# Optimization experiments

Hardware: AMD Instinct MI355X
Metric: run time of the kernel (lower is better)

## Reference

```python
import jax, jax.numpy as jnp
import numpy as np

B, T, D = 128, 512, 512
K = 64  # memory slots per bank


def setup_inputs() -> dict:
    key = jax.random.key(0)
    ks = jax.random.split(key, 8)
    stdv = 1.0 / np.sqrt(D)
    return {
        "x": jax.random.normal(ks[0], (B, T, D), jnp.float32),
        "Amem": jax.random.uniform(ks[1], (K, D), jnp.float32, -stdv, stdv),
        "Nmem": jax.random.uniform(ks[2], (K, D), jnp.float32, -stdv, stdv),
        "W_mu": jax.random.normal(ks[3], (D, D), jnp.float32) * 0.02,
        "b_mu": jnp.zeros((D,), jnp.float32),
        "W_var": jax.random.normal(ks[4], (D, D), jnp.float32) * 0.02,
        "b_var": jnp.zeros((D,), jnp.float32),
        # reparameterization noise (torch.randn_like(std)), shape of N_aug: [B//2, T, D]
        "epsilon": jax.random.normal(ks[5], (B // 2, T, D), jnp.float32),
    }


def _memory(data, mem):
    # UR-DMU / DA-MIST Memory_Bank: sigmoid attention over memory slots
    att = jax.nn.sigmoid(jnp.einsum('btd,kd->btk', data, mem)
                         / jnp.sqrt(jnp.asarray(mem.shape[-1], data.dtype)))
    topv, _ = jax.lax.top_k(att, mem.shape[0] // 16 + 1)   # [b,t,k']
    t_att = topv.mean(-1)                                  # [b,t]
    aug = jnp.einsum('btk,kd->btd', att, mem)              # [b,t,d]
    return t_att, aug


def _l2norm(v):
    return v / jnp.linalg.norm(v, axis=-1, keepdims=True)


def _gather_mean(feats, idx):
    # feats [b,t,d], idx [b,k] -> mean over gathered snippets -> [b,d]
    return jnp.take_along_axis(feats, idx[:, :, None], axis=1).mean(1)


def reference(x, Amem, Nmem, W_mu, b_mu, W_var, b_var, epsilon):
    b, t, d = x.shape
    mid = b // 2
    N_x, A_x = x[:mid], x[mid:]

    A_att, A_aug = _memory(A_x, Amem)
    N_Aatt, N_Aaug = _memory(A_x, Nmem)
    A_Natt, A_Naug = _memory(N_x, Amem)
    N_att, N_aug = _memory(N_x, Nmem)

    k = t // 16 + 1
    _, A_idx = jax.lax.top_k(A_att, k)   # [mid,k]
    _, N_idx = jax.lax.top_k(N_att, k)
    _, P_idx = jax.lax.top_k(N_Aatt, k)

    negative_ax = _gather_mean(A_x, A_idx)
    anchor_nx = _gather_mean(N_x, N_idx)
    positive_nx = _gather_mean(A_x, P_idx)

    a, p, n = _l2norm(anchor_nx), _l2norm(positive_nx), _l2norm(negative_ax)
    # torch TripletMarginLoss: pairwise_distance adds eps=1e-6 elementwise
    d_ap = jnp.linalg.norm(a - p + 1e-6, axis=-1)
    d_an = jnp.linalg.norm(a - n + 1e-6, axis=-1)
    triplet = jnp.mean(jnp.maximum(d_ap - d_an + 1.0, 0.0))

    mu_fn = lambda h: h @ W_mu + b_mu
    var_fn = lambda h: h @ W_var + b_var

    N_aug_mu = mu_fn(N_aug)
    N_aug_var = var_fn(N_aug)
    N_aug_new = N_aug_mu + epsilon * jnp.sqrt(jnp.exp(N_aug_var))

    anchor_nx_new = _gather_mean(N_aug_new, N_idx)    # reshape(mid,1,-1).mean(1) is identity
    A_aug_new = mu_fn(A_aug)
    negative_ax_new = _gather_mean(A_aug_new, A_idx)

    kl_loss = jnp.mean(-0.5 * jnp.sum(1.0 + N_aug_var - N_aug_mu ** 2 - jnp.exp(N_aug_var), axis=1))

    A_Naug_mu = mu_fn(A_Naug)
    N_Aaug_mu = mu_fn(N_Aaug)

    distance = jnp.mean(jax.nn.relu(100.0
                                    - jnp.linalg.norm(negative_ax_new, axis=-1)
                                    + jnp.linalg.norm(anchor_nx_new, axis=-1)))

    F_M = jnp.concatenate(
        [x, jnp.concatenate([N_aug_new + A_Naug_mu, A_aug_new + N_Aaug_mu], axis=0)],
        axis=-1)  # [b,t,2d]

    return (F_M, triplet, kl_loss, distance, A_att, N_att, A_Natt, N_Aatt)
```

## Files before the change

### kernel.cpp

```cpp
#include <hip/hip_runtime.h>
#include <hip/hip_bf16.h>
#include <math.h>

typedef unsigned short u16;
typedef __attribute__((ext_vector_type(4))) float f32x4;
typedef __attribute__((ext_vector_type(8))) short s16x8;

#define O_FM    0ULL
#define O_TRIP  67108864ULL
#define O_KL    67108865ULL
#define O_DIST  67108866ULL
#define O_AATT  67108867ULL
#define O_NATT  67141635ULL
#define O_ANATT 67174403ULL
#define O_NAATT 67207171ULL

#define WS_ATTB  0ULL
#define WS_BCT   16777216ULL
#define WS_PVT   16908288ULL
#define WS_PAM   16973824ULL
#define WS_PNM   17104896ULL
#define WS_PNV   17235968ULL
#define WS_MBH   17367040ULL
#define WS_MBL   17498112ULL
#define WS_TATT  17629184ULL
#define WS_IDX   18022400ULL
#define WS_GATH  18053120ULL
#define WS_NORM  18446336ULL
#define WS_KL    18446848ULL
#define WS_TRIPB 18447360ULL
#define WS_SUM   18447616ULL

__device__ __forceinline__ u16 f2bf(float f) {
    union { float f; unsigned int u; } c; c.f = f;
    unsigned int r = c.u + 0x7fffu + ((c.u >> 16) & 1u);
    return (u16)(r >> 16);
}
__device__ __forceinline__ float bf2f(u16 h) {
    union { unsigned int u; float f; } c; c.u = ((unsigned int)h) << 16;
    return c.f;
}

__device__ __forceinline__ float blk_sum(float v, float* red) {
    #pragma unroll
    for (int o = 32; o; o >>= 1) v += __shfl_xor(v, o);
    int tid = threadIdx.x;
    if ((tid & 63) == 0) red[tid >> 6] = v;
    __syncthreads();
    float r = red[0] + red[1] + red[2] + red[3];
    __syncthreads();
    return r;
}

__device__ __forceinline__ float blk_sum8(float v, float* red, int tid) {
    #pragma unroll
    for (int o = 32; o; o >>= 1) v += __shfl_xor(v, o);
    if ((tid & 63) == 0) red[tid >> 6] = v;
    __syncthreads();
    float r = red[0];
    #pragma unroll
    for (int i = 1; i < 8; ++i) r += red[i];
    __syncthreads();
    return r;
}

__device__ __forceinline__ void stage32_512(const u16* __restrict__ g, int row0, int ld, int k0,
                                            u16* s, int tid) {
    const u16* src = g + (size_t)(row0 + (tid >> 2)) * ld + k0 + (tid & 3) * 8;
    __builtin_amdgcn_global_load_lds((const __attribute__((address_space(1))) void*)src,
                                     (__attribute__((address_space(3))) void*)(s + tid * 8),
                                     16, 0, 0);
}

__global__ __launch_bounds__(256) void k_pp(const float* __restrict__ Amem, const float* __restrict__ Nmem,
                                            const float* __restrict__ Wmu, const float* __restrict__ Wvar,
                                            char* __restrict__ ws) {
    __shared__ float mr[512];
    int bid = blockIdx.x, tid = threadIdx.x;
    if (bid < 256) {
        int i = bid * 256 + tid;
        if (i == 0) *(float*)(ws + WS_KL) = 0.f;
        if (i < 32768) ((float*)(ws + WS_SUM))[i] = 0.f;
        int k = i >> 9, d = i & 511;
        float v = (k < 64) ? Amem[(size_t)k * 512 + d] : Nmem[(size_t)(k - 64) * 512 + d];
        u16 h = f2bf(v);
        ((u16*)(ws + WS_MBH))[i] = h;
        ((u16*)(ws + WS_MBL))[i] = f2bf(v - bf2f(h));
        return;
    }
    int pb = bid - 256;
    float* pam = (float*)(ws + WS_PAM);
    float* pnm = (float*)(ws + WS_PNM);
    float* pnv = (float*)(ws + WS_PNV);
    u16* bct = (u16*)(ws + WS_BCT);
    u16* pvt = (u16*)(ws + WS_PVT);
    int mat = pb >> 6, k = pb & 63;
    const float* mrow = ((mat == 0) ? Amem : Nmem) + (size_t)k * 512;
    const float* W = (mat == 2) ? Wvar : Wmu;
    mr[tid] = mrow[tid]; mr[tid + 256] = mrow[tid + 256];
    __syncthreads();
    float s0 = 0.f, s1 = 0.f;
    for (int d = 0; d < 512; ++d) {
        float m = mr[d];
        s0 += m * W[(size_t)d * 512 + tid];
        s1 += m * W[(size_t)d * 512 + tid + 256];
    }
    if (mat == 0) {
        pam[(size_t)k * 512 + tid] = s0; pam[(size_t)k * 512 + tid + 256] = s1;
        bct[(size_t)tid * 128 + k] = f2bf(s0); bct[(size_t)(tid + 256) * 128 + k] = f2bf(s1);
    } else if (mat == 1) {
        pnm[(size_t)k * 512 + tid] = s0; pnm[(size_t)k * 512 + tid + 256] = s1;
        bct[(size_t)tid * 128 + 64 + k] = f2bf(s0); bct[(size_t)(tid + 256) * 128 + 64 + k] = f2bf(s1);
    } else {
        pnv[(size_t)k * 512 + tid] = s0; pnv[(size_t)k * 512 + tid + 256] = s1;
        pvt[(size_t)tid * 64 + k] = f2bf(s0); pvt[(size_t)(tid + 256) * 64 + k] = f2bf(s1);
    }
}

__global__ __launch_bounds__(512) void k_dots(const float* __restrict__ x, char* __restrict__ ws,
                                              float* __restrict__ out) {
    __shared__ u16 sXh[128 * 32];
    __shared__ u16 sXl[128 * 32];
    __shared__ u16 sBh[128 * 32];
    __shared__ u16 sBl[128 * 32];

    int tid = threadIdx.x;
    int row0 = blockIdx.x * 128;
    const u16* mbh = (const u16*)(ws + WS_MBH);
    const u16* mbl = (const u16*)(ws + WS_MBL);
    u16* attb = (u16*)(ws + WS_ATTB);
    int lane = tid & 63, wid = tid >> 6;
    int cl = lane & 15, rq = lane >> 4;

    f32x4 acc[8];
    #pragma unroll
    for (int i = 0; i < 8; ++i) acc[i] = (f32x4)0.f;

    for (int dc = 0; dc < 16; ++dc) {
        int d0 = dc * 32;
        {
            int r = tid >> 2, q4 = tid & 3;
            const float* sp = x + (size_t)(row0 + r) * 512 + d0 + q4 * 8;
            float* op = out + (size_t)(row0 + r) * 1024 + d0 + q4 * 8;
            f32x4 v0 = *(const f32x4*)(sp);
            f32x4 v1 = *(const f32x4*)(sp + 4);
            *(f32x4*)(op) = v0;
            *(f32x4*)(op + 4) = v1;
            s16x8 hs, ls;
            #pragma unroll
            for (int j = 0; j < 4; ++j) {
                u16 h0 = f2bf(v0[j]); hs[j] = (short)h0; ls[j] = (short)f2bf(v0[j] - bf2f(h0));
                u16 h1 = f2bf(v1[j]); hs[4 + j] = (short)h1; ls[4 + j] = (short)f2bf(v1[j] - bf2f(h1));
            }
            *(s16x8*)&sXh[r * 32 + q4 * 8] = hs;
            *(s16x8*)&sXl[r * 32 + q4 * 8] = ls;
        }
        stage32_512(mbh, 0, 512, d0, sBh, tid);
        stage32_512(mbl, 0, 512, d0, sBl, tid);
        __syncthreads();
        s16x8 axh = *(const s16x8*)&sXh[(wid * 16 + cl) * 32 + rq * 8];
        s16x8 axl = *(const s16x8*)&sXl[(wid * 16 + cl) * 32 + rq * 8];
        #pragma unroll
        for (int ni = 0; ni < 8; ++ni) {
            s16x8 bh = *(const s16x8*)&sBh[(ni * 16 + cl) * 32 + rq * 8];
            s16x8 bl = *(const s16x8*)&sBl[(ni * 16 + cl) * 32 + rq * 8];
            acc[ni] = __builtin_amdgcn_mfma_f32_16x16x32_bf16(axh, bh, acc[ni], 0, 0, 0);
            acc[ni] = __builtin_amdgcn_mfma_f32_16x16x32_bf16(axh, bl, acc[ni], 0, 0, 0);
            acc[ni] = __builtin_amdgcn_mfma_f32_16x16x32_bf16(axl, bh, acc[ni], 0, 0, 0);
        }
        __syncthreads();
    }

    #pragma unroll
    for (int ni = 0; ni < 8; ++ni) {
        #pragma unroll
        for (int q = 0; q < 4; ++q) {
            float logit = acc[ni][q] * 0.044194173824159216f;
            float av = 1.f / (1.f + expf(-logit));
            acc[ni][q] = av;
            attb[(size_t)(row0 + wid * 16 + rq * 4 + q) * 128 + ni * 16 + cl] = f2bf(av);
        }
    }

    unsigned long long gmask = 0xFFFFull << (lane & 48);
    float* tatt = (float*)(ws + WS_TATT);
    int half = row0 >> 15;
    #pragma unroll
    for (int q = 0; q < 4; ++q) {
        #pragma unroll
        for (int side = 0; side < 2; ++side) {
            float v0 = acc[side * 4 + 0][q], v1 = acc[side * 4 + 1][q];
            float v2 = acc[side * 4 + 2][q], v3 = acc[side * 4 + 3][q];
            float sum5 = 0.f;
            #pragma unroll
            for (int it = 0; it < 5; ++it) {
                float m = v0; int jm = 0;
                if (v1 > m) { m = v1; jm = 1; }
                if (v2 > m) { m = v2; jm = 2; }
                if (v3 > m) { m = v3; jm = 3; }
                float g = m;
                g = fmaxf(g, __shfl_xor(g, 1));
                g = fmaxf(g, __shfl_xor(g, 2));
                g = fmaxf(g, __shfl_xor(g, 4));
                g = fmaxf(g, __shfl_xor(g, 8));
                sum5 += g;
                unsigned long long bl = __ballot(m == g) & gmask;
                int owner = __ffsll(bl) - 1;
                if (lane == owner) {
                    if (jm == 0) v0 = -INFINITY;
                    else if (jm == 1) v1 = -INFINITY;
                    else if (jm == 2) v2 = -INFINITY;
                    else v3 = -INFINITY;
                }
            }
            if (cl == 0) {
                float tv = sum5 / 5.f;
                int lr = (row0 + wid * 16 + rq * 4 + q) & 32767;
                if (half) {
                    if (side == 0) { out[O_AATT + lr]  = tv; tatt[lr] = tv; }
                    else           { out[O_NAATT + lr] = tv; tatt[2 * 32768 + lr] = tv; }
                } else {
                    if (side == 0) { out[O_ANATT + lr] = tv; }
                    else           { out[O_NATT + lr]  = tv; tatt[32768 + lr] = tv; }
                }
            }
        }
    }
}

__global__ __launch_bounds__(256) void k_tg(const float* __restrict__ tatt, int* __restrict__ idx,
                                            const float* __restrict__ x, float* __restrict__ gath) {
    __shared__ float vals[512];
    __shared__ int il[40];
    int s = blockIdx.x >> 6, b = blockIdx.x & 63, tid = threadIdx.x;
    const float* src = tatt + (size_t)s * 32768 + b * 512;
    vals[tid] = src[tid]; vals[tid + 256] = src[tid + 256];
    __syncthreads();
    #pragma unroll
    for (int e = 0; e < 2; ++e) {
        int i = tid + e * 256;
        float v = vals[i];
        int rank = 0;
        for (int j = 0; j < 512; j += 4) {
            f32x4 w4 = *(const f32x4*)&vals[j];
            rank += (w4.x > v) || (w4.x == v && (j + 0) < i);
            rank += (w4.y > v) || (w4.y == v && (j + 1) < i);
            rank += (w4.z > v) || (w4.z == v && (j + 2) < i);
            rank += (w4.w > v) || (w4.w == v && (j + 3) < i);
        }
        if (rank < 33) { idx[(s * 64 + b) * 40 + rank] = i; il[rank] = i; }
    }
    __syncthreads();
    int srcb = (s == 1) ? b : 64 + b;
    const float* xb = x + (size_t)srcb * 262144;
    int d0 = tid * 2;
    float a0 = 0.f, a1 = 0.f;
    for (int i = 0; i < 33; ++i) {
        const float* p = xb + (size_t)il[i] * 512 + d0;
        a0 += p[0]; a1 += p[1];
    }
    gath[((size_t)s * 64 + b) * 512 + d0]     = a0 / 33.f;
    gath[((size_t)s * 64 + b) * 512 + d0 + 1] = a1 / 33.f;
}

__device__ __forceinline__ void body_G1(char* smem, int m0, int c0, int tid,
                                        const u16* __restrict__ attb, const u16* __restrict__ bct,
                                        const u16* __restrict__ pvt, const float* __restrict__ bmu,
                                        const float* __restrict__ bvar, const float* __restrict__ epsv,
                                        float* __restrict__ fm, float* __restrict__ klacc) {
    u16* sAA = (u16*)(smem);
    u16* sAN = (u16*)(smem + 8192);
    u16* sBA = (u16*)(smem + 16384);
    u16* sBN = (u16*)(smem + 24576);
    u16* sBV = (u16*)(smem + 32768);
    float* red = (float*)(smem + 40960);
    int lane = tid & 63, wid = tid >> 6;
    int wr = wid >> 2, wc = wid & 3;
    int cl = lane & 15, rq = lane >> 4;

    f32x4 aA[4][2], aN[4][2], aV[4][2];
    #pragma unroll
    for (int i = 0; i < 4; ++i)
        #pragma unroll
        for (int j = 0; j < 2; ++j) { aA[i][j] = (f32x4)0.f; aN[i][j] = (f32x4)0.f; aV[i][j] = (f32x4)0.f; }

    for (int kt = 0; kt < 2; ++kt) {
        stage32_512(attb, m0, 128, kt * 32, sAA, tid);
        stage32_512(attb, m0, 128, 64 + kt * 32, sAN, tid);
        stage32_512(bct, c0, 128, kt * 32, sBA, tid);
        stage32_512(bct, c0, 128, 64 + kt * 32, sBN, tid);
        stage32_512(pvt, c0, 64, kt * 32, sBV, tid);
        __syncthreads();
        s16x8 fA[4], fN[4], bA[2], bN[2], bV[2];
        #pragma unroll
        for (int i = 0; i < 4; ++i) {
            fA[i] = *(const s16x8*)&sAA[(wr * 64 + i * 16 + cl) * 32 + rq * 8];
            fN[i] = *(const s16x8*)&sAN[(wr * 64 + i * 16 + cl) * 32 + rq * 8];
        }
        #pragma unroll
        for (int n = 0; n < 2; ++n) {
            bA[n] = *(const s16x8*)&sBA[(wc * 32 + n * 16 + cl) * 32 + rq * 8];
            bN[n] = *(const s16x8*)&sBN[(wc * 32 + n * 16 + cl) * 32 + rq * 8];
            bV[n] = *(const s16x8*)&sBV[(wc * 32 + n * 16 + cl) * 32 + rq * 8];
        }
        #pragma unroll
        for (int mi = 0; mi < 4; ++mi)
            #pragma unroll
            for (int ni = 0; ni < 2; ++ni) {
                aA[mi][ni] = __builtin_amdgcn_mfma_f32_16x16x32_bf16(fA[mi], bA[ni], aA[mi][ni], 0, 0, 0);
                aN[mi][ni] = __builtin_amdgcn_mfma_f32_16x16x32_bf16(fN[mi], bN[ni], aN[mi][ni], 0, 0, 0);
                aV[mi][ni] = __builtin_amdgcn_mfma_f32_16x16x32_bf16(fN[mi], bV[ni], aV[mi][ni], 0, 0, 0);
            }
        __syncthreads();
    }

    float kll = 0.f;
    #pragma unroll
    for (int mi = 0; mi < 4; ++mi)
        #pragma unroll
        for (int ni = 0; ni < 2; ++ni) {
            int col = c0 + wc * 32 + ni * 16 + cl;
            int rowb = m0 + wr * 64 + mi * 16 + rq * 4;
            float bm = bmu[col], bv = bvar[col];
            #pragma unroll
            for (int q = 0; q < 4; ++q) {
                int row = rowb + q;
                float muN = aN[mi][ni][q] + bm;
                float var = aV[mi][ni][q] + bv;
                float ev = expf(var);
                float muA = aA[mi][ni][q] + bm;
                fm[(size_t)row * 1024 + 512 + col] =
                    muN + epsv[(size_t)row * 512 + col] * sqrtf(ev) + muA;
                kll += 1.f + var - muN * muN - ev;
            }
        }
    #pragma unroll
    for (int o = 32; o; o >>= 1) kll += __shfl_xor(kll, o);
    if (lane == 0) red[wid] = kll;
    __syncthreads();
    if (tid == 0) {
        float s = 0.f;
        #pragma unroll
        for (int i = 0; i < 8; ++i) s += red[i];
        atomicAdd(klacc, s);
    }
}

__device__ __forceinline__ void body_G3(char* smem, int m0, int c0, int tid,
                                        const u16* __restrict__ attb, const u16* __restrict__ bct,
                                        const float* __restrict__ bmu, float* __restrict__ fm) {
    u16* sA = (u16*)(smem);
    u16* sB = (u16*)(smem + 8192);
    int lane = tid & 63, wid = tid >> 6;
    int wr = wid >> 2, wc = wid & 3;
    int cl = lane & 15, rq = lane >> 4;

    f32x4 acc[4][2];
    #pragma unroll
    for (int i = 0; i < 4; ++i)
        #pragma unroll
        for (int j = 0; j < 2; ++j) acc[i][j] = (f32x4)0.f;

    for (int kt = 0; kt < 4; ++kt) {
        stage32_512(attb, 32768 + m0, 128, kt * 32, sA, tid);
        stage32_512(bct, c0, 128, kt * 32, sB, tid);
        __syncthreads();
        s16x8 fa[4], fb[2];
        #pragma unroll
        for (int i = 0; i < 4; ++i)
            fa[i] = *(const s16x8*)&sA[(wr * 64 + i * 16 + cl) * 32 + rq * 8];
        #pragma unroll
        for (int n = 0; n < 2; ++n)
            fb[n] = *(const s16x8*)&sB[(wc * 32 + n * 16 + cl) * 32 + rq * 8];
        #pragma unroll
        for (int mi = 0; mi < 4; ++mi)
            #pragma unroll
            for (int ni = 0; ni < 2; ++ni)
                acc[mi][ni] = __builtin_amdgcn_mfma_f32_16x16x32_bf16(fa[mi], fb[ni], acc[mi][ni], 0, 0, 0);
        __syncthreads();
    }
    #pragma unroll
    for (int mi = 0; mi < 4; ++mi)
        #pragma unroll
        for (int ni = 0; ni < 2; ++ni) {
            int col = c0 + wc * 32 + ni * 16 + cl;
            int rowb = 32768 + m0 + wr * 64 + mi * 16 + rq * 4;
            float bm2 = 2.f * bmu[col];
            #pragma unroll
            for (int q = 0; q < 4; ++q)
                fm[(size_t)(rowb + q) * 1024 + 512 + col] = acc[mi][ni][q] + bm2;
        }
}

__device__ __forceinline__ void body_g2a(char* smem, int blk, int tid,
                                         const int* __restrict__ idx, const u16* __restrict__ attb,
                                         const float* __restrict__ pnm, const float* __restrict__ pnv,
                                         const float* __restrict__ bmu, const float* __restrict__ bvar,
                                         const float* __restrict__ epsv, float* __restrict__ SUM) {
    float* arow = (float*)smem;
    int b = blk / 3, seg = blk % 3;
    float s0 = 0.f, s1 = 0.f;
    for (int i = seg * 11; i < seg * 11 + 11; ++i) {
        int t = idx[(64 + b) * 40 + i];
        size_t r = (size_t)b * 512 + t;
        __syncthreads();
        if (tid < 64) arow[tid] = bf2f(attb[r * 128 + 64 + tid]);
        __syncthreads();
        if (tid < 256) {
            float mu0 = bmu[tid], mu1 = bmu[tid + 256];
            float v0 = bvar[tid], v1 = bvar[tid + 256];
            for (int k = 0; k < 64; ++k) {
                float a = arow[k];
                mu0 += a * pnm[(size_t)k * 512 + tid];
                mu1 += a * pnm[(size_t)k * 512 + tid + 256];
                v0  += a * pnv[(size_t)k * 512 + tid];
                v1  += a * pnv[(size_t)k * 512 + tid + 256];
            }
            s0 += mu0 + bf2f(f2bf(0.f)) + epsv[r * 512 + tid]       * sqrtf(expf(v0));
            s1 += mu1 + epsv[r * 512 + tid + 256] * sqrtf(expf(v1));
        }
    }
    if (tid < 256) {
        atomicAdd(&SUM[(size_t)b * 512 + tid], s0);
        atomicAdd(&SUM[(size_t)b * 512 + tid + 256], s1);
    }
}

__device__ __forceinline__ void body_g2b(char* smem, int b, int tid,
                                         const int* __restrict__ idx, const u16* __restrict__ attb,
                                         const float* __restrict__ pam, const float* __restrict__ bmu,
                                         float* __restrict__ norms) {
    float* meanA = (float*)smem;
    float* red = (float*)(smem + 256);
    if (tid < 64) {
        float s = 0.f;
        for (int i = 0; i < 33; ++i) {
            int t = idx[b * 40 + i];
            s += bf2f(attb[(size_t)(32768 + b * 512 + t) * 128 + tid]);
        }
        meanA[tid] = s * (1.f / 33.f);
    }
    __syncthreads();
    float ssv = 0.f;
    if (tid < 256) {
        float s0 = bmu[tid], s1 = bmu[tid + 256];
        #pragma unroll 4
        for (int k = 0; k < 64; ++k) {
            float m = meanA[k];
            s0 += m * pam[(size_t)k * 512 + tid];
            s1 += m * pam[(size_t)k * 512 + tid + 256];
        }
        ssv = s0 * s0 + s1 * s1;
    }
    float ss = blk_sum8(ssv, red, tid);
    if (tid == 0) norms[64 + b] = sqrtf(ss);
}

__global__ __launch_bounds__(512) void k_post(const u16* __restrict__ attb, const u16* __restrict__ bct,
                                              const u16* __restrict__ pvt, const float* __restrict__ bmu,
                                              const float* __restrict__ bvar, const float* __restrict__ epsv,
                                              const int* __restrict__ idx, const float* __restrict__ pam,
                                              const float* __restrict__ pnm, const float* __restrict__ pnv,
                                              float* __restrict__ fm, float* __restrict__ klacc,
                                              float* __restrict__ SUM, float* __restrict__ norms) {
    __shared__ __align__(16) char smem[41024];
    int bid = blockIdx.x, tid = threadIdx.x;
    if (bid < 1024) {
        body_G1(smem, (bid >> 2) * 128, (bid & 3) * 128, tid, attb, bct, pvt, bmu, bvar, epsv, fm, klacc);
    } else if (bid < 2048) {
        int b2 = bid - 1024;
        body_G3(smem, (b2 >> 2) * 128, (b2 & 3) * 128, tid, attb, bct, bmu, fm);
    } else if (bid < 2240) {
        body_g2a(smem, bid - 2048, tid, idx, attb, pnm, pnv, bmu, bvar, epsv, SUM);
    } else {
        body_g2b(smem, bid - 2240, tid, idx, attb, pam, bmu, norms);
    }
}

__global__ __launch_bounds__(256) void k_nt(const float* __restrict__ SUM, const float* __restrict__ gath,
                                            float* __restrict__ norms, float* __restrict__ tripb) {
    __shared__ float red[8];
    int bid = blockIdx.x, tid = threadIdx.x;
    if (bid < 64) {
        int b = bid;
        float s0 = SUM[(size_t)b * 512 + tid] / 33.f;
        float s1 = SUM[(size_t)b * 512 + tid + 256] / 33.f;
        float ss = blk_sum(s0 * s0 + s1 * s1, red);
        if (tid == 0) norms[b] = sqrtf(ss);
    } else {
        int b = bid - 64;
        const float* a = gath + (size_t)(64 + b) * 512;
        const float* p = gath + (size_t)(128 + b) * 512;
        const float* n = gath + (size_t)(b) * 512;
        float a0 = a[tid], a1 = a[tid + 256];
        float p0 = p[tid], p1 = p[tid + 256];
        float n0 = n[tid], n1 = n[tid + 256];
        float na  = sqrtf(blk_sum(a0 * a0 + a1 * a1, red));
        float npv = sqrtf(blk_sum(p0 * p0 + p1 * p1, red));
        float nn  = sqrtf(blk_sum(n0 * n0 + n1 * n1, red));
        float e0 = a0 / na - p0 / npv + 1e-6f, e1 = a1 / na - p1 / npv + 1e-6f;
        float f0 = a0 / na - n0 / nn  + 1e-6f, f1 = a1 / na - n1 / nn  + 1e-6f;
        float dap = sqrtf(blk_sum(e0 * e0 + e1 * e1, red));
        float dan = sqrtf(blk_sum(f0 * f0 + f1 * f1, red));
        if (tid == 0) tripb[b] = fmaxf(dap - dan + 1.f, 0.f);
    }
}

__global__ __launch_bounds__(64) void k_final(const float* __restrict__ norms, const float* __restrict__ klacc,
                                              const float* __restrict__ tripb, float* __restrict__ out) {
    int tid = threadIdx.x;
    float v = fmaxf(100.f - norms[64 + tid] + norms[tid], 0.f);
    float t = tripb[tid];
    #pragma unroll
    for (int o = 32; o; o >>= 1) { v += __shfl_xor(v, o); t += __shfl_xor(t, o); }
    if (tid == 0) {
        out[O_DIST] = v / 64.f;
        out[O_TRIP] = t / 64.f;
        out[O_KL]   = -0.5f * (*klacc) / 32768.f;
    }
}

extern "C" void kernel_launch(void* const* d_in, const int* in_sizes, int n_in,
                              void* d_out, int out_size, void* d_ws, size_t ws_size,
                              hipStream_t stream) {
    const float* x    = (const float*)d_in[0];
    const float* Amem = (const float*)d_in[1];
    const float* Nmem = (const float*)d_in[2];
    const float* Wmu  = (const float*)d_in[3];
    const float* bmu  = (const float*)d_in[4];
    const float* Wvar = (const float*)d_in[5];
    const float* bvar = (const float*)d_in[6];
    const float* eps  = (const float*)d_in[7];
    float* out = (float*)d_out;
    char* ws = (char*)d_ws;
    const u16* attb  = (const u16*)(ws + WS_ATTB);
    const u16* bct   = (const u16*)(ws + WS_BCT);
    const u16* pvt   = (const u16*)(ws + WS_PVT);
    const float* pam = (const float*)(ws + WS_PAM);
    const float* pnm = (const float*)(ws + WS_PNM);
    const float* pnv = (const float*)(ws + WS_PNV);
    const int* idx   = (const int*)(ws + WS_IDX);

    k_pp<<<448, 256, 0, stream>>>(Amem, Nmem, Wmu, Wvar, ws);
    k_dots<<<512, 512, 0, stream>>>(x, ws, out);
    k_tg<<<192, 256, 0, stream>>>((const float*)(ws + WS_TATT), (int*)(ws + WS_IDX), x,
                                  (float*)(ws + WS_GATH));
    k_post<<<2304, 512, 0, stream>>>(attb, bct, pvt, bmu, bvar, eps, idx, pam, pnm, pnv,
                                     out, (float*)(ws + WS_KL), (float*)(ws + WS_SUM),
                                     (float*)(ws + WS_NORM));
    k_nt<<<128, 256, 0, stream>>>((const float*)(ws + WS_SUM), (const float*)(ws + WS_GATH),
                                  (float*)(ws + WS_NORM), (float*)(ws + WS_TRIPB));
    k_final<<<1, 64, 0, stream>>>((const float*)(ws + WS_NORM), (const float*)(ws + WS_KL),
                                  (const float*)(ws + WS_TRIPB), out);
}
```

Baseline: 272.4 us.

## Fuse norm, triplet and final reductions into k_post; widen k_dots K-chunk

Removes the k_nt and k_final launches. Per-batch norms now run in the last-arriving g2a block, found with an atomic counter; the triplet blocks are appended to k_post; and the final scalar reduction runs in the globally last block, selected by a second atomic counter. Separately, k_dots now stages 64-wide K chunks instead of 32, which halves the number of barrier iterations but doubles shared memory use. The changes save two launch gaps and some synchronisation, in exchange for atomics and threadfences in every k_post block and possible lower occupancy in k_dots.

```diff
diff --git a/kernel.cpp b/kernel.cpp
--- a/kernel.cpp
+++ b/kernel.cpp
@@ -30,6 +30,10 @@
 #define WS_KL    18446848ULL
 #define WS_TRIPB 18447360ULL
 #define WS_SUM   18447616ULL
+#define WS_CNTB  18578688ULL
+#define WS_GCNT  18578944ULL
+
+#define NPOST 2368
 
 __device__ __forceinline__ u16 f2bf(float f) {
     union { float f; unsigned int u; } c; c.f = f;
@@ -39,17 +43,6 @@
 __device__ __forceinline__ float bf2f(u16 h) {
     union { unsigned int u; float f; } c; c.u = ((unsigned int)h) << 16;
     return c.f;
-}
-
-__device__ __forceinline__ float blk_sum(float v, float* red) {
-    #pragma unroll
-    for (int o = 32; o; o >>= 1) v += __shfl_xor(v, o);
-    int tid = threadIdx.x;
-    if ((tid & 63) == 0) red[tid >> 6] = v;
-    __syncthreads();
-    float r = red[0] + red[1] + red[2] + red[3];
-    __syncthreads();
-    return r;
 }
 
 __device__ __forceinline__ float blk_sum8(float v, float* red, int tid) {
@@ -70,6 +63,16 @@
     __builtin_amdgcn_global_load_lds((const __attribute__((address_space(1))) void*)src,
                                      (__attribute__((address_space(3))) void*)(s + tid * 8),
                                      16, 0, 0);
+}
+
+__device__ __forceinline__ void stage64_512(const u16* __restrict__ g, int d0, u16* s, int tid) {
+    #pragma unroll
+    for (int j = 0; j < 2; ++j) {
+        const u16* src = g + (size_t)(j * 64 + (tid >> 3)) * 512 + d0 + (tid & 7) * 8;
+        __builtin_amdgcn_global_load_lds((const __attribute__((address_space(1))) void*)src,
+                                         (__attribute__((address_space(3))) void*)(s + j * 4096 + tid * 8),
+                                         16, 0, 0);
+    }
 }
 
 __global__ __launch_bounds__(256) void k_pp(const float* __restrict__ Amem, const float* __restrict__ Nmem,
@@ -79,7 +82,8 @@
     int bid = blockIdx.x, tid = threadIdx.x;
     if (bid < 256) {
         int i = bid * 256 + tid;
-        if (i == 0) *(float*)(ws + WS_KL) = 0.f;
+        if (i == 0) { *(float*)(ws + WS_KL) = 0.f; *(int*)(ws + WS_GCNT) = 0; }
+        if (bid == 0 && tid < 64) ((int*)(ws + WS_CNTB))[tid] = 0;
         if (i < 32768) ((float*)(ws + WS_SUM))[i] = 0.f;
         int k = i >> 9, d = i & 511;
         float v = (k < 64) ? Amem[(size_t)k * 512 + d] : Nmem[(size_t)(k - 64) * 512 + d];
@@ -119,10 +123,10 @@
 
 __global__ __launch_bounds__(512) void k_dots(const float* __restrict__ x, char* __restrict__ ws,
                                               float* __restrict__ out) {
-    __shared__ u16 sXh[128 * 32];
-    __shared__ u16 sXl[128 * 32];
-    __shared__ u16 sBh[128 * 32];
-    __shared__ u16 sBl[128 * 32];
+    __shared__ u16 sXh[128 * 64];
+    __shared__ u16 sXl[128 * 64];
+    __shared__ u16 sBh[128 * 64];
+    __shared__ u16 sBl[128 * 64];
 
     int tid = threadIdx.x;
     int row0 = blockIdx.x * 128;
@@ -136,37 +140,46 @@
     #pragma unroll
     for (int i = 0; i < 8; ++i) acc[i] = (f32x4)0.f;
 
-    for (int dc = 0; dc < 16; ++dc) {
-        int d0 = dc * 32;
+    for (int dc = 0; dc < 8; ++dc) {
+        int d0 = dc * 64;
         {
             int r = tid >> 2, q4 = tid & 3;
-            const float* sp = x + (size_t)(row0 + r) * 512 + d0 + q4 * 8;
-            float* op = out + (size_t)(row0 + r) * 1024 + d0 + q4 * 8;
+            const float* sp = x + (size_t)(row0 + r) * 512 + d0 + q4 * 16;
+            float* op = out + (size_t)(row0 + r) * 1024 + d0 + q4 * 16;
             f32x4 v0 = *(const f32x4*)(sp);
             f32x4 v1 = *(const f32x4*)(sp + 4);
-            *(f32x4*)(op) = v0;
-            *(f32x4*)(op + 4) = v1;
-            s16x8 hs, ls;
+            f32x4 v2 = *(const f32x4*)(sp + 8);
+            f32x4 v3 = *(const f32x4*)(sp + 12);
+            *(f32x4*)(op) = v0; *(f32x4*)(op + 4) = v1;
+            *(f32x4*)(op + 8) = v2; *(f32x4*)(op + 12) = v3;
+            s16x8 h0, l0, h1, l1;
             #pragma unroll
             for (int j = 0; j < 4; ++j) {
-                u16 h0 = f2bf(v0[j]); hs[j] = (short)h0; ls[j] = (short)f2bf(v0[j] - bf2f(h0));
-                u16 h1 = f2bf(v1[j]); hs[4 + j] = (short)h1; ls[4 + j] = (short)f2bf(v1[j] - bf2f(h1));
-            }
-            *(s16x8*)&sXh[r * 32 + q4 * 8] = hs;
-            *(s16x8*)&sXl[r * 32 + q4 * 8] = ls;
-        }
-        stage32_512(mbh, 0, 512, d0, sBh, tid);
-        stage32_512(mbl, 0, 512, d0, sBl, tid);
-        __syncthreads();
-        s16x8 axh = *(const s16x8*)&sXh[(wid * 16 + cl) * 32 + rq * 8];
-        s16x8 axl = *(const s16x8*)&sXl[(wid * 16 + cl) * 32 + rq * 8];
-        #pragma unroll
-        for (int ni = 0; ni < 8; ++ni) {
-            s16x8 bh = *(const s16x8*)&sBh[(ni * 16 + cl) * 32 + rq * 8];
-            s16x8 bl = *(const s16x8*)&sBl[(ni * 16 + cl) * 32 + rq * 8];
-            acc[ni] = __builtin_amdgcn_mfma_f32_16x16x32_bf16(axh, bh, acc[ni], 0, 0, 0);
-            acc[ni] = __builtin_amdgcn_mfma_f32_16x16x32_bf16(axh, bl, acc[ni], 0, 0, 0);
-            acc[ni] = __builtin_amdgcn_mfma_f32_16x16x32_bf16(axl, bh, acc[ni], 0, 0, 0);
+                u16 a = f2bf(v0[j]); h0[j] = (short)a; l0[j] = (short)f2bf(v0[j] - bf2f(a));
+                u16 b = f2bf(v1[j]); h0[4 + j] = (short)b; l0[4 + j] = (short)f2bf(v1[j] - bf2f(b));
+                u16 c = f2bf(v2[j]); h1[j] = (short)c; l1[j] = (short)f2bf(v2[j] - bf2f(c));
+                u16 d = f2bf(v3[j]); h1[4 + j] = (short)d; l1[4 + j] = (short)f2bf(v3[j] - bf2f(d));
+            }
+            *(s16x8*)&sXh[r * 64 + q4 * 16]     = h0;
+            *(s16x8*)&sXh[r * 64 + q4 * 16 + 8] = h1;
+            *(s16x8*)&sXl[r * 64 + q4 * 16]     = l0;
+            *(s16x8*)&sXl[r * 64 + q4 * 16 + 8] = l1;
+        }
+        stage64_512(mbh, d0, sBh, tid);
+        stage64_512(mbl, d0, sBl, tid);
+        __syncthreads();
+        #pragma unroll
+        for (int kk = 0; kk < 2; ++kk) {
+            s16x8 axh = *(const s16x8*)&sXh[(wid * 16 + cl) * 64 + kk * 32 + rq * 8];
+            s16x8 axl = *(const s16x8*)&sXl[(wid * 16 + cl) * 64 + kk * 32 + rq * 8];
+            #pragma unroll
+            for (int ni = 0; ni < 8; ++ni) {
+                s16x8 bh = *(const s16x8*)&sBh[(ni * 16 + cl) * 64 + kk * 32 + rq * 8];
+                s16x8 bl = *(const s16x8*)&sBl[(ni * 16 + cl) * 64 + kk * 32 + rq * 8];
+                acc[ni] = __builtin_amdgcn_mfma_f32_16x16x32_bf16(axh, bh, acc[ni], 0, 0, 0);
+                acc[ni] = __builtin_amdgcn_mfma_f32_16x16x32_bf16(axh, bl, acc[ni], 0, 0, 0);
+                acc[ni] = __builtin_amdgcn_mfma_f32_16x16x32_bf16(axl, bh, acc[ni], 0, 0, 0);
+            }
         }
         __syncthreads();
     }
@@ -416,7 +429,7 @@
                 v0  += a * pnv[(size_t)k * 512 + tid];
                 v1  += a * pnv[(size_t)k * 512 + tid + 256];
             }
-            s0 += mu0 + bf2f(f2bf(0.f)) + epsv[r * 512 + tid]       * sqrtf(expf(v0));
+            s0 += mu0 + epsv[r * 512 + tid]       * sqrtf(expf(v0));
             s1 += mu1 + epsv[r * 512 + tid + 256] * sqrtf(expf(v1));
         }
     }
@@ -456,14 +469,56 @@
     if (tid == 0) norms[64 + b] = sqrtf(ss);
 }
 
+__device__ __forceinline__ void body_norm2a(char* smem, int b, int tid,
+                                            const float* __restrict__ SUM, float* __restrict__ norms) {
+    float* red = (float*)smem;
+    float v = 0.f;
+    if (tid < 256) {
+        float s0 = SUM[(size_t)b * 512 + tid] / 33.f;
+        float s1 = SUM[(size_t)b * 512 + tid + 256] / 33.f;
+        v = s0 * s0 + s1 * s1;
+    }
+    float ss = blk_sum8(v, red, tid);
+    if (tid == 0) norms[b] = sqrtf(ss);
+}
+
+__device__ __forceinline__ void body_trip(char* smem, int b, int tid,
+                                          const float* __restrict__ gath, float* __restrict__ tripb) {
+    float* red = (float*)smem;
+    const float* a = gath + (size_t)(64 + b) * 512;
+    const float* p = gath + (size_t)(128 + b) * 512;
+    const float* n = gath + (size_t)(b) * 512;
+    float a0 = 0.f, a1 = 0.f, p0 = 0.f, p1 = 0.f, n0 = 0.f, n1 = 0.f;
+    if (tid < 256) {
+        a0 = a[tid]; a1 = a[tid + 256];
+        p0 = p[tid]; p1 = p[tid + 256];
+        n0 = n[tid]; n1 = n[tid + 256];
+    }
+    float na  = sqrtf(blk_sum8(tid < 256 ? a0 * a0 + a1 * a1 : 0.f, red, tid));
+    float npv = sqrtf(blk_sum8(tid < 256 ? p0 * p0 + p1 * p1 : 0.f, red, tid));
+    float nn  = sqrtf(blk_sum8(tid < 256 ? n0 * n0 + n1 * n1 : 0.f, red, tid));
+    float e0 = 0.f, e1 = 0.f, f0 = 0.f, f1 = 0.f;
+    if (tid < 256) {
+        e0 = a0 / na - p0 / npv + 1e-6f; e1 = a1 / na - p1 / npv + 1e-6f;
+        f0 = a0 / na - n0 / nn  + 1e-6f; f1 = a1 / na - n1 / nn  + 1e-6f;
+    }
+    float dap = sqrtf(blk_sum8(tid < 256 ? e0 * e0 + e1 * e1 : 0.f, red, tid));
+    float dan = sqrtf(blk_sum8(tid < 256 ? f0 * f0 + f1 * f1 : 0.f, red, tid));
+    if (tid == 0) tripb[b] = fmaxf(dap - dan + 1.f, 0.f);
+}
+
 __global__ __launch_bounds__(512) void k_post(const u16* __restrict__ attb, const u16* __restrict__ bct,
                                               const u16* __restrict__ pvt, const float* __restrict__ bmu,
                                               const float* __restrict__ bvar, const float* __restrict__ epsv,
                                               const int* __restrict__ idx, const float* __restrict__ pam,
                                               const float* __restrict__ pnm, const float* __restrict__ pnv,
+                                              const float* __restrict__ gath,
                                               float* __restrict__ fm, float* __restrict__ klacc,
-                                              float* __restrict__ SUM, float* __restrict__ norms) {
+                                              float* __restrict__ SUM, float* __restrict__ norms,
+                                              float* __restrict__ tripb, int* __restrict__ cntb,
+                                              int* __restrict__ gcnt, float* __restrict__ out) {
     __shared__ __align__(16) char smem[41024];
+    __shared__ int sflag;
     int bid = blockIdx.x, tid = threadIdx.x;
     if (bid < 1024) {
         body_G1(smem, (bid >> 2) * 128, (bid & 3) * 128, tid, attb, bct, pvt, bmu, bvar, epsv, fm, klacc);
@@ -471,52 +526,36 @@
         int b2 = bid - 1024;
         body_G3(smem, (b2 >> 2) * 128, (b2 & 3) * 128, tid, attb, bct, bmu, fm);
     } else if (bid < 2240) {
-        body_g2a(smem, bid - 2048, tid, idx, attb, pnm, pnv, bmu, bvar, epsv, SUM);
+        int blk = bid - 2048;
+        body_g2a(smem, blk, tid, idx, attb, pnm, pnv, bmu, bvar, epsv, SUM);
+        int b = blk / 3;
+        __threadfence();
+        __syncthreads();
+        if (tid == 0) sflag = (atomicAdd(&cntb[b], 1) == 2) ? 1 : 0;
+        __syncthreads();
+        if (sflag) { __threadfence(); body_norm2a(smem, b, tid, SUM, norms); }
+    } else if (bid < 2304) {
+        body_g2b(smem, bid - 2240, tid, idx, attb, pam, bmu, norms);
     } else {
-        body_g2b(smem, bid - 2240, tid, idx, attb, pam, bmu, norms);
-    }
-}
-
-__global__ __launch_bounds__(256) void k_nt(const float* __restrict__ SUM, const float* __restrict__ gath,
-                                            float* __restrict__ norms, float* __restrict__ tripb) {
-    __shared__ float red[8];
-    int bid = blockIdx.x, tid = threadIdx.x;
-    if (bid < 64) {
-        int b = bid;
-        float s0 = SUM[(size_t)b * 512 + tid] / 33.f;
-        float s1 = SUM[(size_t)b * 512 + tid + 256] / 33.f;
-        float ss = blk_sum(s0 * s0 + s1 * s1, red);
-        if (tid == 0) norms[b] = sqrtf(ss);
-    } else {
-        int b = bid - 64;
-        const float* a = gath + (size_t)(64 + b) * 512;
-        const float* p = gath + (size_t)(128 + b) * 512;
-        const float* n = gath + (size_t)(b) * 512;
-        float a0 = a[tid], a1 = a[tid + 256];
-        float p0 = p[tid], p1 = p[tid + 256];
-        float n0 = n[tid], n1 = n[tid + 256];
-        float na  = sqrtf(blk_sum(a0 * a0 + a1 * a1, red));
-        float npv = sqrtf(blk_sum(p0 * p0 + p1 * p1, red));
-        float nn  = sqrtf(blk_sum(n0 * n0 + n1 * n1, red));
-        float e0 = a0 / na - p0 / npv + 1e-6f, e1 = a1 / na - p1 / npv + 1e-6f;
-        float f0 = a0 / na - n0 / nn  + 1e-6f, f1 = a1 / na - n1 / nn  + 1e-6f;
-        float dap = sqrtf(blk_sum(e0 * e0 + e1 * e1, red));
-        float dan = sqrtf(blk_sum(f0 * f0 + f1 * f1, red));
-        if (tid == 0) tripb[b] = fmaxf(dap - dan + 1.f, 0.f);
-    }
-}
-
-__global__ __launch_bounds__(64) void k_final(const float* __restrict__ norms, const float* __restrict__ klacc,
-                                              const float* __restrict__ tripb, float* __restrict__ out) {
-    int tid = threadIdx.x;
-    float v = fmaxf(100.f - norms[64 + tid] + norms[tid], 0.f);
-    float t = tripb[tid];
-    #pragma unroll
-    for (int o = 32; o; o >>= 1) { v += __shfl_xor(v, o); t += __shfl_xor(t, o); }
-    if (tid == 0) {
-        out[O_DIST] = v / 64.f;
-        out[O_TRIP] = t / 64.f;
-        out[O_KL]   = -0.5f * (*klacc) / 32768.f;
+        body_trip(smem, bid - 2304, tid, gath, tripb);
+    }
+    __threadfence();
+    __syncthreads();
+    if (tid == 0) sflag = (atomicAdd(gcnt, 1) == NPOST - 1) ? 1 : 0;
+    __syncthreads();
+    if (sflag) {
+        __threadfence();
+        if (tid < 64) {
+            float v = fmaxf(100.f - norms[64 + tid] + norms[tid], 0.f);
+            float t = tripb[tid];
+            #pragma unroll
+            for (int o = 32; o; o >>= 1) { v += __shfl_xor(v, o); t += __shfl_xor(t, o); }
+            if (tid == 0) {
+                out[O_DIST] = v / 64.f;
+                out[O_TRIP] = t / 64.f;
+                out[O_KL]   = -0.5f * (*klacc) / 32768.f;
+            }
+        }
     }
 }
 
@@ -545,11 +584,9 @@
     k_dots<<<512, 512, 0, stream>>>(x, ws, out);
     k_tg<<<192, 256, 0, stream>>>((const float*)(ws + WS_TATT), (int*)(ws + WS_IDX), x,
                                   (float*)(ws + WS_GATH));
-    k_post<<<2304, 512, 0, stream>>>(attb, bct, pvt, bmu, bvar, eps, idx, pam, pnm, pnv,
-                                     out, (float*)(ws + WS_KL), (float*)(ws + WS_SUM),
-                                     (float*)(ws + WS_NORM));
-    k_nt<<<128, 256, 0, stream>>>((const float*)(ws + WS_SUM), (const float*)(ws + WS_GATH),
-                                  (float*)(ws + WS_NORM), (float*)(ws + WS_TRIPB));
-    k_final<<<1, 64, 0, stream>>>((const float*)(ws + WS_NORM), (const float*)(ws + WS_KL),
-                                  (const float*)(ws + WS_TRIPB), out);
-}
+    k_post<<<NPOST, 512, 0, stream>>>(attb, bct, pvt, bmu, bvar, eps, idx, pam, pnm, pnv,
+                                      (const float*)(ws + WS_GATH),
+                                      out, (float*)(ws + WS_KL), (float*)(ws + WS_SUM),
+                                      (float*)(ws + WS_NORM), (float*)(ws + WS_TRIPB),
+                                      (int*)(ws + WS_CNTB), (int*)(ws + WS_GCNT), out);
+}
```

After: 784.9 us. 188% more time.

## Merge top-k gather into GEMM launch and regroup dependent post kernels

Applied to the files above, without the earlier changes.

The standalone top-k/gather kernel now runs as extra blocks inside the large GEMM post kernel, so its latency overlaps the GEMM work instead of serializing before it. The index-dependent gathers (g2a, g2b) and the triplet reduction move into a second kernel, and the norm reduction becomes its own small kernel. Launch count stays the same. The top-k blocks now run at 512 threads with half of them idle, and they may be scheduled after the GEMM blocks, which can limit the overlap.

```diff
diff --git a/kernel.cpp b/kernel.cpp
--- a/kernel.cpp
+++ b/kernel.cpp
@@ -228,41 +228,6 @@
     }
 }
 
-__global__ __launch_bounds__(256) void k_tg(const float* __restrict__ tatt, int* __restrict__ idx,
-                                            const float* __restrict__ x, float* __restrict__ gath) {
-    __shared__ float vals[512];
-    __shared__ int il[40];
-    int s = blockIdx.x >> 6, b = blockIdx.x & 63, tid = threadIdx.x;
-    const float* src = tatt + (size_t)s * 32768 + b * 512;
-    vals[tid] = src[tid]; vals[tid + 256] = src[tid + 256];
-    __syncthreads();
-    #pragma unroll
-    for (int e = 0; e < 2; ++e) {
-        int i = tid + e * 256;
-        float v = vals[i];
-        int rank = 0;
-        for (int j = 0; j < 512; j += 4) {
-            f32x4 w4 = *(const f32x4*)&vals[j];
-            rank += (w4.x > v) || (w4.x == v && (j + 0) < i);
-            rank += (w4.y > v) || (w4.y == v && (j + 1) < i);
-            rank += (w4.z > v) || (w4.z == v && (j + 2) < i);
-            rank += (w4.w > v) || (w4.w == v && (j + 3) < i);
-        }
-        if (rank < 33) { idx[(s * 64 + b) * 40 + rank] = i; il[rank] = i; }
-    }
-    __syncthreads();
-    int srcb = (s == 1) ? b : 64 + b;
-    const float* xb = x + (size_t)srcb * 262144;
-    int d0 = tid * 2;
-    float a0 = 0.f, a1 = 0.f;
-    for (int i = 0; i < 33; ++i) {
-        const float* p = xb + (size_t)il[i] * 512 + d0;
-        a0 += p[0]; a1 += p[1];
-    }
-    gath[((size_t)s * 64 + b) * 512 + d0]     = a0 / 33.f;
-    gath[((size_t)s * 64 + b) * 512 + d0 + 1] = a1 / 33.f;
-}
-
 __device__ __forceinline__ void body_G1(char* smem, int m0, int c0, int tid,
                                         const u16* __restrict__ attb, const u16* __restrict__ bct,
                                         const u16* __restrict__ pvt, const float* __restrict__ bmu,
@@ -392,6 +357,46 @@
         }
 }
 
+__device__ __forceinline__ void body_tg(char* smem, int sb, int tid,
+                                        const float* __restrict__ tatt, int* __restrict__ idx,
+                                        const float* __restrict__ x, float* __restrict__ gath) {
+    float* vals = (float*)smem;
+    int* il = (int*)(smem + 2048);
+    int s = sb >> 6, b = sb & 63;
+    const float* src = tatt + (size_t)s * 32768 + b * 512;
+    if (tid < 256) { vals[tid] = src[tid]; vals[tid + 256] = src[tid + 256]; }
+    __syncthreads();
+    if (tid < 256) {
+        #pragma unroll
+        for (int e = 0; e < 2; ++e) {
+            int i = tid + e * 256;
+            float v = vals[i];
+            int rank = 0;
+            for (int j = 0; j < 512; j += 4) {
+                f32x4 w4 = *(const f32x4*)&vals[j];
+                rank += (w4.x > v) || (w4.x == v && (j + 0) < i);
+                rank += (w4.y > v) || (w4.y == v && (j + 1) < i);
+                rank += (w4.z > v) || (w4.z == v && (j + 2) < i);
+                rank += (w4.w > v) || (w4.w == v && (j + 3) < i);
+            }
+            if (rank < 33) { idx[(s * 64 + b) * 40 + rank] = i; il[rank] = i; }
+        }
+    }
+    __syncthreads();
+    if (tid < 256) {
+        int srcb = (s == 1) ? b : 64 + b;
+        const float* xb = x + (size_t)srcb * 262144;
+        int d0 = tid * 2;
+        float a0 = 0.f, a1 = 0.f;
+        for (int i = 0; i < 33; ++i) {
+            const float* p = xb + (size_t)il[i] * 512 + d0;
+            a0 += p[0]; a1 += p[1];
+        }
+        gath[((size_t)s * 64 + b) * 512 + d0]     = a0 / 33.f;
+        gath[((size_t)s * 64 + b) * 512 + d0 + 1] = a1 / 33.f;
+    }
+}
+
 __device__ __forceinline__ void body_g2a(char* smem, int blk, int tid,
                                          const int* __restrict__ idx, const u16* __restrict__ attb,
                                          const float* __restrict__ pnm, const float* __restrict__ pnv,
@@ -416,7 +421,7 @@
                 v0  += a * pnv[(size_t)k * 512 + tid];
                 v1  += a * pnv[(size_t)k * 512 + tid + 256];
             }
-            s0 += mu0 + bf2f(f2bf(0.f)) + epsv[r * 512 + tid]       * sqrtf(expf(v0));
+            s0 += mu0 + epsv[r * 512 + tid]       * sqrtf(expf(v0));
             s1 += mu1 + epsv[r * 512 + tid + 256] * sqrtf(expf(v1));
         }
     }
@@ -456,13 +461,37 @@
     if (tid == 0) norms[64 + b] = sqrtf(ss);
 }
 
-__global__ __launch_bounds__(512) void k_post(const u16* __restrict__ attb, const u16* __restrict__ bct,
-                                              const u16* __restrict__ pvt, const float* __restrict__ bmu,
-                                              const float* __restrict__ bvar, const float* __restrict__ epsv,
-                                              const int* __restrict__ idx, const float* __restrict__ pam,
-                                              const float* __restrict__ pnm, const float* __restrict__ pnv,
-                                              float* __restrict__ fm, float* __restrict__ klacc,
-                                              float* __restrict__ SUM, float* __restrict__ norms) {
+__device__ __forceinline__ void body_trip(char* smem, int b, int tid,
+                                          const float* __restrict__ gath, float* __restrict__ tripb) {
+    float* red = (float*)smem;
+    const float* a = gath + (size_t)(64 + b) * 512;
+    const float* p = gath + (size_t)(128 + b) * 512;
+    const float* n = gath + (size_t)(b) * 512;
+    float a0 = 0.f, a1 = 0.f, p0 = 0.f, p1 = 0.f, n0 = 0.f, n1 = 0.f;
+    if (tid < 256) {
+        a0 = a[tid]; a1 = a[tid + 256];
+        p0 = p[tid]; p1 = p[tid + 256];
+        n0 = n[tid]; n1 = n[tid + 256];
+    }
+    float na  = sqrtf(blk_sum8(tid < 256 ? a0 * a0 + a1 * a1 : 0.f, red, tid));
+    float npv = sqrtf(blk_sum8(tid < 256 ? p0 * p0 + p1 * p1 : 0.f, red, tid));
+    float nn  = sqrtf(blk_sum8(tid < 256 ? n0 * n0 + n1 * n1 : 0.f, red, tid));
+    float e0 = 0.f, e1 = 0.f, f0 = 0.f, f1 = 0.f;
+    if (tid < 256) {
+        e0 = a0 / na - p0 / npv + 1e-6f; e1 = a1 / na - p1 / npv + 1e-6f;
+        f0 = a0 / na - n0 / nn  + 1e-6f; f1 = a1 / na - n1 / nn  + 1e-6f;
+    }
+    float dap = sqrtf(blk_sum8(tid < 256 ? e0 * e0 + e1 * e1 : 0.f, red, tid));
+    float dan = sqrtf(blk_sum8(tid < 256 ? f0 * f0 + f1 * f1 : 0.f, red, tid));
+    if (tid == 0) tripb[b] = fmaxf(dap - dan + 1.f, 0.f);
+}
+
+__global__ __launch_bounds__(512) void k_postA(const u16* __restrict__ attb, const u16* __restrict__ bct,
+                                               const u16* __restrict__ pvt, const float* __restrict__ bmu,
+                                               const float* __restrict__ bvar, const float* __restrict__ epsv,
+                                               const float* __restrict__ tatt, int* __restrict__ idx,
+                                               const float* __restrict__ x, float* __restrict__ gath,
+                                               float* __restrict__ fm, float* __restrict__ klacc) {
     __shared__ __align__(16) char smem[41024];
     int bid = blockIdx.x, tid = threadIdx.x;
     if (bid < 1024) {
@@ -470,40 +499,35 @@
     } else if (bid < 2048) {
         int b2 = bid - 1024;
         body_G3(smem, (b2 >> 2) * 128, (b2 & 3) * 128, tid, attb, bct, bmu, fm);
-    } else if (bid < 2240) {
-        body_g2a(smem, bid - 2048, tid, idx, attb, pnm, pnv, bmu, bvar, epsv, SUM);
     } else {
-        body_g2b(smem, bid - 2240, tid, idx, attb, pam, bmu, norms);
-    }
-}
-
-__global__ __launch_bounds__(256) void k_nt(const float* __restrict__ SUM, const float* __restrict__ gath,
-                                            float* __restrict__ norms, float* __restrict__ tripb) {
+        body_tg(smem, bid - 2048, tid, tatt, idx, x, gath);
+    }
+}
+
+__global__ __launch_bounds__(512) void k_postB(const int* __restrict__ idx, const u16* __restrict__ attb,
+                                               const float* __restrict__ pam, const float* __restrict__ pnm,
+                                               const float* __restrict__ pnv, const float* __restrict__ bmu,
+                                               const float* __restrict__ bvar, const float* __restrict__ epsv,
+                                               const float* __restrict__ gath, float* __restrict__ SUM,
+                                               float* __restrict__ norms, float* __restrict__ tripb) {
+    __shared__ __align__(16) char smem[2304];
+    int bid = blockIdx.x, tid = threadIdx.x;
+    if (bid < 192) {
+        body_g2a(smem, bid, tid, idx, attb, pnm, pnv, bmu, bvar, epsv, SUM);
+    } else if (bid < 256) {
+        body_g2b(smem, bid - 192, tid, idx, attb, pam, bmu, norms);
+    } else {
+        body_trip(smem, bid - 256, tid, gath, tripb);
+    }
+}
+
+__global__ __launch_bounds__(256) void k_norm2a(const float* __restrict__ SUM, float* __restrict__ norms) {
     __shared__ float red[8];
-    int bid = blockIdx.x, tid = threadIdx.x;
-    if (bid < 64) {
-        int b = bid;
-        float s0 = SUM[(size_t)b * 512 + tid] / 33.f;
-        float s1 = SUM[(size_t)b * 512 + tid + 256] / 33.f;
-        float ss = blk_sum(s0 * s0 + s1 * s1, red);
-        if (tid == 0) norms[b] = sqrtf(ss);
-    } else {
-        int b = bid - 64;
-        const float* a = gath + (size_t)(64 + b) * 512;
-        const float* p = gath + (size_t)(128 + b) * 512;
-        const float* n = gath + (size_t)(b) * 512;
-        float a0 = a[tid], a1 = a[tid + 256];
-        float p0 = p[tid], p1 = p[tid + 256];
-        float n0 = n[tid], n1 = n[tid + 256];
-        float na  = sqrtf(blk_sum(a0 * a0 + a1 * a1, red));
-        float npv = sqrtf(blk_sum(p0 * p0 + p1 * p1, red));
-        float nn  = sqrtf(blk_sum(n0 * n0 + n1 * n1, red));
-        float e0 = a0 / na - p0 / npv + 1e-6f, e1 = a1 / na - p1 / npv + 1e-6f;
-        float f0 = a0 / na - n0 / nn  + 1e-6f, f1 = a1 / na - n1 / nn  + 1e-6f;
-        float dap = sqrtf(blk_sum(e0 * e0 + e1 * e1, red));
-        float dan = sqrtf(blk_sum(f0 * f0 + f1 * f1, red));
-        if (tid == 0) tripb[b] = fmaxf(dap - dan + 1.f, 0.f);
-    }
+    int b = blockIdx.x, tid = threadIdx.x;
+    float s0 = SUM[(size_t)b * 512 + tid] / 33.f;
+    float s1 = SUM[(size_t)b * 512 + tid + 256] / 33.f;
+    float ss = blk_sum(s0 * s0 + s1 * s1, red);
+    if (tid == 0) norms[b] = sqrtf(ss);
 }
 
 __global__ __launch_bounds__(64) void k_final(const float* __restrict__ norms, const float* __restrict__ klacc,
@@ -543,13 +567,13 @@
 
     k_pp<<<448, 256, 0, stream>>>(Amem, Nmem, Wmu, Wvar, ws);
     k_dots<<<512, 512, 0, stream>>>(x, ws, out);
-    k_tg<<<192, 256, 0, stream>>>((const float*)(ws + WS_TATT), (int*)(ws + WS_IDX), x,
-                                  (float*)(ws + WS_GATH));
-    k_post<<<2304, 512, 0, stream>>>(attb, bct, pvt, bmu, bvar, eps, idx, pam, pnm, pnv,
-                                     out, (float*)(ws + WS_KL), (float*)(ws + WS_SUM),
-                                     (float*)(ws + WS_NORM));
-    k_nt<<<128, 256, 0, stream>>>((const float*)(ws + WS_SUM), (const float*)(ws + WS_GATH),
-                                  (float*)(ws + WS_NORM), (float*)(ws + WS_TRIPB));
+    k_postA<<<2240, 512, 0, stream>>>(attb, bct, pvt, bmu, bvar, eps,
+                                      (const float*)(ws + WS_TATT), (int*)(ws + WS_IDX), x,
+                                      (float*)(ws + WS_GATH), out, (float*)(ws + WS_KL));
+    k_postB<<<320, 512, 0, stream>>>(idx, attb, pam, pnm, pnv, bmu, bvar, eps,
+                                     (const float*)(ws + WS_GATH), (float*)(ws + WS_SUM),
+                                     (float*)(ws + WS_NORM), (float*)(ws + WS_TRIPB));
+    k_norm2a<<<64, 256, 0, stream>>>((const float*)(ws + WS_SUM), (float*)(ws + WS_NORM));
     k_final<<<1, 64, 0, stream>>>((const float*)(ws + WS_NORM), (const float*)(ws + WS_KL),
                                   (const float*)(ws + WS_TRIPB), out);
 }
```

Result: no change. 273.7 us (+0.5%).
